# Kernel optimization log

Measured on AMD Instinct MI355X. Metric: run time of the kernel, lower is better.

## Reference

```python
import jax, jax.numpy as jnp
import numpy as np

N, E, IN, HID, OUT, H = 50000, 400000, 128, 32, 64, 4
HID_DIM = HID * H  # 128


def _param(key, shape, scale=0.05):
    return jax.random.normal(key, shape, dtype=jnp.float32) * scale


def setup_inputs() -> dict:
    key = jax.random.key(0)
    ks = jax.random.split(key, 32)
    inp = {
        "x": jax.random.normal(ks[0], (N, IN), dtype=jnp.float32),
        "edge_index": jax.random.randint(ks[1], (2, E), 0, N, dtype=jnp.int32),
        "edge_weight": jax.random.uniform(ks[2], (E,), dtype=jnp.float32),
        # layer 0: in=128 -> H=4, C=32, concat => 128
        "Wl0": _param(ks[3], (IN, H * HID)), "bl0": jnp.zeros((H * HID,), jnp.float32),
        "Wr0": _param(ks[4], (IN, H * HID)), "br0": jnp.zeros((H * HID,), jnp.float32),
        "We0": _param(ks[5], (1, H * HID)),
        "att0": _param(ks[6], (H, HID)),
        "b0": jnp.zeros((H * HID,), jnp.float32),
        "g0": jnp.ones((H * HID,), jnp.float32), "be0": jnp.zeros((H * HID,), jnp.float32),
        # layer 1: in=128 -> H=4, C=64, concat=False (mean over heads) => 64
        "Wl1": _param(ks[7], (HID_DIM, H * OUT)), "bl1": jnp.zeros((H * OUT,), jnp.float32),
        "Wr1": _param(ks[8], (HID_DIM, H * OUT)), "br1": jnp.zeros((H * OUT,), jnp.float32),
        "We1": _param(ks[9], (1, H * OUT)),
        "att1": _param(ks[10], (H, OUT)),
        "b1": jnp.zeros((OUT,), jnp.float32),
        "g1": jnp.ones((OUT,), jnp.float32), "be1": jnp.zeros((OUT,), jnp.float32),
        # residual projections
        "P0": _param(ks[11], (IN, HID_DIM)), "pb0": jnp.zeros((HID_DIM,), jnp.float32),
        "P1": _param(ks[12], (HID_DIM, OUT)), "pb1": jnp.zeros((OUT,), jnp.float32),
    }
    return inp


def _add_self_loops(src, dst, ew):
    # PyG add_self_loops with fill_value='mean': loop attr = mean of incoming edge attrs per node
    s = jax.ops.segment_sum(ew, dst, num_segments=N)
    cnt = jax.ops.segment_sum(jnp.ones_like(ew), dst, num_segments=N)
    loop_w = s / jnp.maximum(cnt, 1.0)
    idx = jnp.arange(N, dtype=src.dtype)
    return jnp.concatenate([src, idx]), jnp.concatenate([dst, idx]), jnp.concatenate([ew, loop_w])


def _gatv2_layer(x, src, dst, ew, Wl, bl, Wr, br, We, att, b, g, be, C, concat):
    xl = (x @ Wl + bl).reshape(N, H, C)  # source transform (lin_l)
    xr = (x @ Wr + br).reshape(N, H, C)  # target transform (lin_r)
    eattr = (ew[:, None] @ We).reshape(-1, H, C)
    e = jax.nn.leaky_relu(xl[src] + xr[dst] + eattr, 0.2)  # [E', H, C]
    logits = jnp.einsum('ehc,hc->eh', e, att)
    # segment softmax over target nodes
    m = jax.ops.segment_max(logits, dst, num_segments=N)
    p = jnp.exp(logits - m[dst])
    denom = jax.ops.segment_sum(p, dst, num_segments=N)
    alpha = p / denom[dst]
    out = jax.ops.segment_sum(xl[src] * alpha[..., None], dst, num_segments=N)  # [N, H, C]
    if concat:
        out = out.reshape(N, H * C) + b
    else:
        out = out.mean(axis=1) + b
    out = jax.nn.elu(out)
    mu = out.mean(-1, keepdims=True)
    var = out.var(-1, keepdims=True)
    return (out - mu) / jnp.sqrt(var + 1e-5) * g + be


def reference(x, edge_index, edge_weight,
              Wl0, bl0, Wr0, br0, We0, att0, b0, g0, be0,
              Wl1, bl1, Wr1, br1, We1, att1, b1, g1, be1,
              P0, pb0, P1, pb1):
    src, dst, ew = _add_self_loops(edge_index[0], edge_index[1], edge_weight)
    h = x
    h1 = _gatv2_layer(h, src, dst, ew, Wl0, bl0, Wr0, br0, We0, att0, b0, g0, be0, HID, True)
    h = h1 + (h @ P0 + pb0)
    h2 = _gatv2_layer(h, src, dst, ew, Wl1, bl1, Wr1, br1, We1, att1, b1, g1, be1, OUT, False)
    h = h2 + (h @ P1 + pb1)
    return h
```

## Files before the change

kernel.cpp:

```cpp
#include <hip/hip_runtime.h>
#include <math.h>

#define N_NODES 50000
#define N_EDGES 400000
#define NPAD    50176
#define MROWS   50048
#define HC0 128
#define HC1 256
#define CSR_TOTAL (N_NODES + N_EDGES)

typedef short    bf16x8 __attribute__((ext_vector_type(8)));
typedef float    f32x4  __attribute__((ext_vector_type(4)));
typedef _Float16 h2     __attribute__((ext_vector_type(2)));
typedef _Float16 h4     __attribute__((ext_vector_type(4)));
typedef _Float16 h8     __attribute__((ext_vector_type(8)));

__device__ inline unsigned short f2bf(float f) {
  union { float f; unsigned u; } v; v.f = f;
  unsigned r = v.u + 0x7FFFu + ((v.u >> 16) & 1u);
  return (unsigned short)(r >> 16);
}
__device__ inline h2 mkh2(float a, float b) {
  h2 r; r[0] = (_Float16)a; r[1] = (_Float16)b; return r;
}
__device__ inline float hdot2(h2 a, h2 b, float c) {
#if __has_builtin(__builtin_amdgcn_fdot2)
  return __builtin_amdgcn_fdot2(a, b, c, false);
#else
  return c + (float)a[0] * (float)b[0] + (float)a[1] * (float)b[1];
#endif
}

__global__ void deg_kernel(const int* __restrict__ ei, const float* __restrict__ ew,
                           float* __restrict__ s, int* __restrict__ deg) {
  int e = blockIdx.x * 256 + threadIdx.x;
  if (e < N_EDGES) {
    int dst = ei[N_EDGES + e];
    atomicAdd(&s[dst], ew[e]);
    atomicAdd(&deg[dst], 1);
  }
}

__global__ void scan1(const int* __restrict__ deg, int* __restrict__ part,
                      int* __restrict__ bsum) {
  int i = blockIdx.x * 256 + threadIdx.x;
  int lane = threadIdx.x & 63, wid = threadIdx.x >> 6;
  int v = (i < N_NODES) ? deg[i] + 1 : 0;
  int inc = v;
#pragma unroll
  for (int d = 1; d < 64; d <<= 1) { int y = __shfl_up(inc, d, 64); if (lane >= d) inc += y; }
  __shared__ int wsum[4];
  if (lane == 63) wsum[wid] = inc;
  __syncthreads();
  int off = 0;
#pragma unroll
  for (int w = 0; w < 4; ++w) { int sv = wsum[w]; if (w < wid) off += sv; }
  part[i] = inc - v + off;
  if (threadIdx.x == 0) bsum[blockIdx.x] = wsum[0] + wsum[1] + wsum[2] + wsum[3];
}

__global__ void scan2(int* __restrict__ bsum) {
  int t = threadIdx.x;
  int lane = t & 63, wid = t >> 6;
  int v = (t < 196) ? bsum[t] : 0;
  int inc = v;
#pragma unroll
  for (int d = 1; d < 64; d <<= 1) { int y = __shfl_up(inc, d, 64); if (lane >= d) inc += y; }
  __shared__ int wsum[4];
  if (lane == 63) wsum[wid] = inc;
  __syncthreads();
  int off = 0;
#pragma unroll
  for (int w = 0; w < 4; ++w) { int sv = wsum[w]; if (w < wid) off += sv; }
  if (t < 196) bsum[t] = inc - v + off;
}

__global__ void self_kernel(const float* __restrict__ s, const int* __restrict__ deg,
                            const int* __restrict__ part, const int* __restrict__ bsum,
                            int2* __restrict__ csr2) {
  int i = blockIdx.x * 256 + threadIdx.x;
  if (i >= N_NODES) return;
  float w = s[i] / fmaxf((float)deg[i], 1.0f);
  int start = part[i] + bsum[i >> 8];
  csr2[start] = make_int2(i, __float_as_int(w));
}

__global__ void scatter_kernel(const int* __restrict__ ei, const float* __restrict__ ew,
                               const int* __restrict__ part, const int* __restrict__ bsum,
                               int* __restrict__ cursor, int2* __restrict__ csr2) {
  int e = blockIdx.x * 256 + threadIdx.x;
  if (e >= N_EDGES) return;
  int dst = ei[N_EDGES + e];
  int pos = atomicAdd(&cursor[dst], 1);
  int idx = part[dst] + bsum[dst >> 8] + 1 + pos;
  csr2[idx] = make_int2(ei[e], __float_as_int(ew[e]));
}

__global__ void pack_w(const float* __restrict__ Wl0, const float* __restrict__ Wr0,
                       const float* __restrict__ P0,  const float* __restrict__ Wl1,
                       const float* __restrict__ Wr1, const float* __restrict__ P1,
                       unsigned short* __restrict__ o_wl0, unsigned short* __restrict__ o_wr0,
                       unsigned short* __restrict__ o_p0,  unsigned short* __restrict__ o_wl1,
                       unsigned short* __restrict__ o_wr1, unsigned short* __restrict__ o_p1) {
  int n = blockIdx.x, k = threadIdx.x;
  const float* W; unsigned short* O; int N, nl;
  if      (n < 128) { W = Wl0; O = o_wl0; N = 128; nl = n; }
  else if (n < 256) { W = Wr0; O = o_wr0; N = 128; nl = n - 128; }
  else if (n < 384) { W = P0;  O = o_p0;  N = 128; nl = n - 256; }
  else if (n < 640) { W = Wl1; O = o_wl1; N = 256; nl = n - 384; }
  else if (n < 896) { W = Wr1; O = o_wr1; N = 256; nl = n - 640; }
  else              { W = P1;  O = o_p1;  N = 64;  nl = n - 896; }
  O[nl * 128 + k] = f2bf(W[(size_t)k * N + nl]);
}

__global__ __launch_bounds__(256) void gemm_l0(
    const float* __restrict__ X, const unsigned short* __restrict__ BT,
    const float* __restrict__ bias0, const float* __restrict__ bias1,
    const float* __restrict__ bias2,
    _Float16* __restrict__ o_xl, _Float16* __restrict__ o_xr,
    _Float16* __restrict__ o_h, int M) {
  __shared__ unsigned short As[64 * 136];
  const int tid = threadIdx.x;
  const int rbase = blockIdx.x * 64;
#pragma unroll
  for (int i = 0; i < 8; ++i) {
    int c = i * 256 + tid;
    int row = c >> 5, c4 = c & 31;
    int ar = rbase + row; if (ar > M - 1) ar = M - 1;
    float4 v = *(const float4*)(X + (size_t)ar * 128 + c4 * 4);
    ushort4 o; o.x = f2bf(v.x); o.y = f2bf(v.y); o.z = f2bf(v.z); o.w = f2bf(v.w);
    *(ushort4*)(As + row * 136 + c4 * 4) = o;
  }
  __syncthreads();
  const int w = tid >> 6, l = tid & 63;
  const int lr = l & 15, lg = l >> 4;
#pragma unroll
  for (int i = 0; i < 6; ++i) {
    const int ct = w * 6 + i;
    const bf16x8* bp = (const bf16x8*)(BT + (size_t)(ct * 16 + lr) * 128 + lg * 8);
    bf16x8 b0 = bp[0], b1 = bp[4], b2 = bp[8], b3 = bp[12];
    const int colb = ct * 16 + lg * 4;
    const int cc = colb & 127;
    const float* bptr = (ct < 8 ? bias0 : (ct < 16 ? bias1 : bias2));
    float4 bv = *(const float4*)(bptr + cc);
#pragma unroll
    for (int rt = 0; rt < 4; ++rt) {
      const unsigned short* ap = As + (rt * 16 + lr) * 136 + lg * 8;
      bf16x8 a0 = *(const bf16x8*)(ap);
      bf16x8 a1 = *(const bf16x8*)(ap + 32);
      bf16x8 a2 = *(const bf16x8*)(ap + 64);
      bf16x8 a3 = *(const bf16x8*)(ap + 96);
      f32x4 acc = {0.f, 0.f, 0.f, 0.f};
      acc = __builtin_amdgcn_mfma_f32_16x16x32_bf16(b0, a0, acc, 0, 0, 0);
      acc = __builtin_amdgcn_mfma_f32_16x16x32_bf16(b1, a1, acc, 0, 0, 0);
      acc = __builtin_amdgcn_mfma_f32_16x16x32_bf16(b2, a2, acc, 0, 0, 0);
      acc = __builtin_amdgcn_mfma_f32_16x16x32_bf16(b3, a3, acc, 0, 0, 0);
      const int row = rbase + rt * 16 + lr;
      h4 o;
      o[0] = (_Float16)(acc[0] + bv.x); o[1] = (_Float16)(acc[1] + bv.y);
      o[2] = (_Float16)(acc[2] + bv.z); o[3] = (_Float16)(acc[3] + bv.w);
      _Float16* dst = (ct < 8) ? o_xl : (ct < 16 ? o_xr : o_h);
      *(h4*)(dst + (size_t)row * 128 + cc) = o;
    }
  }
}

__global__ __launch_bounds__(256) void gemm_l1(
    const unsigned short* __restrict__ A, const unsigned short* __restrict__ BT,
    const float* __restrict__ bias0, const float* __restrict__ bias1,
    const float* __restrict__ bias2,
    _Float16* __restrict__ o_xl, _Float16* __restrict__ o_xr,
    float* __restrict__ o_out, int M) {
  __shared__ unsigned short As[64 * 136];
  const int tid = threadIdx.x;
  const int rbase = blockIdx.x * 64;
#pragma unroll
  for (int i = 0; i < 4; ++i) {
    int c = i * 256 + tid;
    int row = c >> 4, slot = c & 15;
    int ar = rbase + row; if (ar > M - 1) ar = M - 1;
    uint4 v = *(const uint4*)(A + (size_t)ar * 128 + slot * 8);
    *(uint4*)(As + row * 136 + slot * 8) = v;
  }
  __syncthreads();
  const int w = tid >> 6, l = tid & 63;
  const int lr = l & 15, lg = l >> 4;
#pragma unroll
  for (int i = 0; i < 9; ++i) {
    const int ct = w * 9 + i;
    const bf16x8* bp = (const bf16x8*)(BT + (size_t)(ct * 16 + lr) * 128 + lg * 8);
    bf16x8 b0 = bp[0], b1 = bp[4], b2 = bp[8], b3 = bp[12];
    const int colb = ct * 16 + lg * 4;
    const int cc = (ct < 32) ? (colb & 255) : (colb - 512);
    const float* bptr = (ct < 16 ? bias0 : (ct < 32 ? bias1 : bias2));
    float4 bv = *(const float4*)(bptr + cc);
#pragma unroll
    for (int rt = 0; rt < 4; ++rt) {
      const unsigned short* ap = As + (rt * 16 + lr) * 136 + lg * 8;
      bf16x8 a0 = *(const bf16x8*)(ap);
      bf16x8 a1 = *(const bf16x8*)(ap + 32);
      bf16x8 a2 = *(const bf16x8*)(ap + 64);
      bf16x8 a3 = *(const bf16x8*)(ap + 96);
      f32x4 acc = {0.f, 0.f, 0.f, 0.f};
      acc = __builtin_amdgcn_mfma_f32_16x16x32_bf16(b0, a0, acc, 0, 0, 0);
      acc = __builtin_amdgcn_mfma_f32_16x16x32_bf16(b1, a1, acc, 0, 0, 0);
      acc = __builtin_amdgcn_mfma_f32_16x16x32_bf16(b2, a2, acc, 0, 0, 0);
      acc = __builtin_amdgcn_mfma_f32_16x16x32_bf16(b3, a3, acc, 0, 0, 0);
      const int row = rbase + rt * 16 + lr;
      if (ct < 32) {
        h4 o;
        o[0] = (_Float16)(acc[0] + bv.x); o[1] = (_Float16)(acc[1] + bv.y);
        o[2] = (_Float16)(acc[2] + bv.z); o[3] = (_Float16)(acc[3] + bv.w);
        *(h4*)((ct < 16 ? o_xl : o_xr) + (size_t)row * 256 + cc) = o;
      } else if (row < M) {
        float4 o;
        o.x = acc[0] + bv.x; o.y = acc[1] + bv.y;
        o.z = acc[2] + bv.z; o.w = acc[3] + bv.w;
        *(float4*)(o_out + (size_t)row * 64 + cc) = o;
      }
    }
  }
}

__device__ inline void edge_step0(int2 rec, h8 a8, bool valid,
                                  const h2* xrv2, const h2* wef2, const h2* att2,
                                  h2* acc2, float& den) {
  _Float16 wh = (_Float16)__int_as_float(rec.y);
  h2 w2; w2[0] = wh; w2[1] = wh;
  const h2 c02 = mkh2(0.2f, 0.2f);
  int4 ai = __builtin_bit_cast(int4, a8);
  h2 av[4];
  av[0] = __builtin_bit_cast(h2, ai.x); av[1] = __builtin_bit_cast(h2, ai.y);
  av[2] = __builtin_bit_cast(h2, ai.z); av[3] = __builtin_bit_cast(h2, ai.w);
  float c = 0.f;
#pragma unroll
  for (int k = 0; k < 4; ++k) {
    h2 sv = av[k] + (w2 * wef2[k] + xrv2[k]);
    h2 lk = __builtin_elementwise_max(sv, sv * c02);
    c = hdot2(lk, att2[k], c);
  }
  c += __shfl_xor(c, 1, 64); c += __shfl_xor(c, 2, 64);
  float p = valid ? __expf(c) : 0.f;
  den += p;
  _Float16 ph = (_Float16)p;
  h2 p2; p2[0] = ph; p2[1] = ph;
#pragma unroll
  for (int k = 0; k < 4; ++k) acc2[k] = p2 * av[k] + acc2[k];
}

__device__ inline void edge_step1(int2 rec, h8 a8, bool valid,
                                  const h2* xrv2, const h2* wef2, const h2* att2,
                                  h2* acc2, float& den) {
  _Float16 wh = (_Float16)__int_as_float(rec.y);
  h2 w2; w2[0] = wh; w2[1] = wh;
  const h2 c02 = mkh2(0.2f, 0.2f);
  int4 ai = __builtin_bit_cast(int4, a8);
  h2 av[4];
  av[0] = __builtin_bit_cast(h2, ai.x); av[1] = __builtin_bit_cast(h2, ai.y);
  av[2] = __builtin_bit_cast(h2, ai.z); av[3] = __builtin_bit_cast(h2, ai.w);
  float c = 0.f;
#pragma unroll
  for (int k = 0; k < 4; ++k) {
    h2 sv = av[k] + (w2 * wef2[k] + xrv2[k]);
    h2 lk = __builtin_elementwise_max(sv, sv * c02);
    c = hdot2(lk, att2[k], c);
  }
  c += __shfl_xor(c, 1, 64); c += __shfl_xor(c, 2, 64); c += __shfl_xor(c, 4, 64);
  float p = valid ? __expf(c) : 0.f;
  den += p;
  _Float16 ph = (_Float16)p;
  h2 p2; p2[0] = ph; p2[1] = ph;
#pragma unroll
  for (int k = 0; k < 4; ++k) acc2[k] = p2 * av[k] + acc2[k];
}

__global__ __launch_bounds__(256) void agg0(
    const int* __restrict__ part, const int* __restrict__ bsum,
    const int* __restrict__ deg, const int2* __restrict__ csr2,
    const _Float16* __restrict__ xl, const _Float16* __restrict__ xr,
    const float* __restrict__ We, const float* __restrict__ att,
    const float* __restrict__ b, const float* __restrict__ g,
    const float* __restrict__ be, const _Float16* __restrict__ hres,
    unsigned short* __restrict__ hout) {
  const int wid = threadIdx.x >> 6, l = threadIdx.x & 63;
  const int n = blockIdx.x * 4 + wid;
  const int grp = l >> 4, cl = l & 15, c0 = cl * 8;
  h2 xrv2[4], wef2[4], att2[4];
  {
    h8 x8 = *(const h8*)(xr + (size_t)n * HC0 + c0);
    int4 xi = __builtin_bit_cast(int4, x8);
    xrv2[0] = __builtin_bit_cast(h2, xi.x); xrv2[1] = __builtin_bit_cast(h2, xi.y);
    xrv2[2] = __builtin_bit_cast(h2, xi.z); xrv2[3] = __builtin_bit_cast(h2, xi.w);
    float4 w0 = *(const float4*)(We + c0),  w1 = *(const float4*)(We + c0 + 4);
    float4 t0 = *(const float4*)(att + c0), t1 = *(const float4*)(att + c0 + 4);
    wef2[0] = mkh2(w0.x, w0.y); wef2[1] = mkh2(w0.z, w0.w);
    wef2[2] = mkh2(w1.x, w1.y); wef2[3] = mkh2(w1.z, w1.w);
    att2[0] = mkh2(t0.x, t0.y); att2[1] = mkh2(t0.z, t0.w);
    att2[2] = mkh2(t1.x, t1.y); att2[3] = mkh2(t1.z, t1.w);
  }
  const int start = part[n] + bsum[n >> 8];
  const int cnt   = deg[n] + 1;
  const int2* seg = csr2 + start;
  h2 acc2[4] = {};
  float den = 0.f;
  int2 rA0 = seg[grp],      rA1 = seg[grp + 4];
  int2 rB0 = seg[grp + 8],  rB1 = seg[grp + 12];
  h8 aA0 = *(const h8*)(xl + (size_t)rA0.x * HC0 + c0);
  h8 aA1 = *(const h8*)(xl + (size_t)rA1.x * HC0 + c0);
  const int trips = (cnt + 7) >> 3;
  int e = grp;
  for (int t = 0; t < trips; ++t) {
    int2 rC0 = seg[e + 16], rC1 = seg[e + 20];
    h8 aB0 = *(const h8*)(xl + (size_t)rB0.x * HC0 + c0);
    h8 aB1 = *(const h8*)(xl + (size_t)rB1.x * HC0 + c0);
    edge_step0(rA0, aA0, e < cnt,     xrv2, wef2, att2, acc2, den);
    edge_step0(rA1, aA1, e + 4 < cnt, xrv2, wef2, att2, acc2, den);
    rA0 = rB0; rA1 = rB1; rB0 = rC0; rB1 = rC1; aA0 = aB0; aA1 = aB1;
    e += 8;
  }
  den += __shfl_xor(den, 16, 64); den += __shfl_xor(den, 32, 64);
#pragma unroll
  for (int k = 0; k < 4; ++k) {
    int b16 = __shfl_xor(__builtin_bit_cast(int, acc2[k]), 16, 64);
    acc2[k] = acc2[k] + __builtin_bit_cast(h2, b16);
    int b32 = __shfl_xor(__builtin_bit_cast(int, acc2[k]), 32, 64);
    acc2[k] = acc2[k] + __builtin_bit_cast(h2, b32);
  }
  float v[8], s1 = 0.f, s2 = 0.f;
  float dinv = 1.f / den;
  {
    float4 b0v = *(const float4*)(b + c0), b1v = *(const float4*)(b + c0 + 4);
    float bb[8] = {b0v.x,b0v.y,b0v.z,b0v.w,b1v.x,b1v.y,b1v.z,b1v.w};
#pragma unroll
    for (int j = 0; j < 8; ++j) {
      float t = (float)acc2[j >> 1][j & 1] * dinv + bb[j];
      t = t > 0.f ? t : __expf(t) - 1.f;
      v[j] = t; s1 += t; s2 += t * t;
    }
  }
  s1 += __shfl_xor(s1, 1, 64); s2 += __shfl_xor(s2, 1, 64);
  s1 += __shfl_xor(s1, 2, 64); s2 += __shfl_xor(s2, 2, 64);
  s1 += __shfl_xor(s1, 4, 64); s2 += __shfl_xor(s2, 4, 64);
  s1 += __shfl_xor(s1, 8, 64); s2 += __shfl_xor(s2, 8, 64);
  float mean = s1 * (1.f / 128.f);
  float inv  = rsqrtf(s2 * (1.f / 128.f) - mean * mean + 1e-5f);
  if (grp == 0) {
    float4 g0v = *(const float4*)(g + c0),  g1v = *(const float4*)(g + c0 + 4);
    float4 e0v = *(const float4*)(be + c0), e1v = *(const float4*)(be + c0 + 4);
    h8 hh = *(const h8*)(hres + (size_t)n * HC0 + c0);
    float gg[8] = {g0v.x,g0v.y,g0v.z,g0v.w,g1v.x,g1v.y,g1v.z,g1v.w};
    float ee[8] = {e0v.x,e0v.y,e0v.z,e0v.w,e1v.x,e1v.y,e1v.z,e1v.w};
    bf16x8 o;
#pragma unroll
    for (int j = 0; j < 8; ++j)
      o[j] = (short)f2bf((v[j] - mean) * inv * gg[j] + ee[j] + (float)hh[j]);
    *(bf16x8*)(hout + (size_t)n * HC0 + c0) = o;
  }
}

__global__ __launch_bounds__(256) void agg1(
    const int* __restrict__ part, const int* __restrict__ bsum,
    const int* __restrict__ deg, const int2* __restrict__ csr2,
    const _Float16* __restrict__ xl, const _Float16* __restrict__ xr,
    const float* __restrict__ We, const float* __restrict__ att,
    const float* __restrict__ b, const float* __restrict__ g,
    const float* __restrict__ be, float* __restrict__ out) {
  const int wid = threadIdx.x >> 6, l = threadIdx.x & 63;
  const int n = blockIdx.x * 4 + wid;
  const int grp = l >> 5, cl = l & 31, c0 = cl * 8;
  h2 xrv2[4], wef2[4], att2[4];
  {
    h8 x8 = *(const h8*)(xr + (size_t)n * HC1 + c0);
    int4 xi = __builtin_bit_cast(int4, x8);
    xrv2[0] = __builtin_bit_cast(h2, xi.x); xrv2[1] = __builtin_bit_cast(h2, xi.y);
    xrv2[2] = __builtin_bit_cast(h2, xi.z); xrv2[3] = __builtin_bit_cast(h2, xi.w);
    float4 w0 = *(const float4*)(We + c0),  w1 = *(const float4*)(We + c0 + 4);
    float4 t0 = *(const float4*)(att + c0), t1 = *(const float4*)(att + c0 + 4);
    wef2[0] = mkh2(w0.x, w0.y); wef2[1] = mkh2(w0.z, w0.w);
    wef2[2] = mkh2(w1.x, w1.y); wef2[3] = mkh2(w1.z, w1.w);
    att2[0] = mkh2(t0.x, t0.y); att2[1] = mkh2(t0.z, t0.w);
    att2[2] = mkh2(t1.x, t1.y); att2[3] = mkh2(t1.z, t1.w);
  }
  const int start = part[n] + bsum[n >> 8];
  const int cnt   = deg[n] + 1;
  const int2* seg = csr2 + start;
  h2 acc2[4] = {};
  float den = 0.f;
  int2 rA0 = seg[grp],     rA1 = seg[grp + 2];
  int2 rB0 = seg[grp + 4], rB1 = seg[grp + 6];
  h8 aA0 = *(const h8*)(xl + (size_t)rA0.x * HC1 + c0);
  h8 aA1 = *(const h8*)(xl + (size_t)rA1.x * HC1 + c0);
  const int trips = (cnt + 3) >> 2;
  int e = grp;
  for (int t = 0; t < trips; ++t) {
    int2 rC0 = seg[e + 8], rC1 = seg[e + 10];
    h8 aB0 = *(const h8*)(xl + (size_t)rB0.x * HC1 + c0);
    h8 aB1 = *(const h8*)(xl + (size_t)rB1.x * HC1 + c0);
    edge_step1(rA0, aA0, e < cnt,     xrv2, wef2, att2, acc2, den);
    edge_step1(rA1, aA1, e + 2 < cnt, xrv2, wef2, att2, acc2, den);
    rA0 = rB0; rA1 = rB1; rB0 = rC0; rB1 = rC1; aA0 = aB0; aA1 = aB1;
    e += 4;
  }
  den += __shfl_xor(den, 32, 64);
#pragma unroll
  for (int k = 0; k < 4; ++k) {
    int b32 = __shfl_xor(__builtin_bit_cast(int, acc2[k]), 32, 64);
    acc2[k] = acc2[k] + __builtin_bit_cast(h2, b32);
  }
  float dinv = 1.f / den;
  float v[8], s1 = 0.f, s2 = 0.f;
  const int oc = (cl & 7) * 8;
  {
    float4 b0v = *(const float4*)(b + oc), b1v = *(const float4*)(b + oc + 4);
    float bb[8] = {b0v.x,b0v.y,b0v.z,b0v.w,b1v.x,b1v.y,b1v.z,b1v.w};
#pragma unroll
    for (int j = 0; j < 8; ++j) {
      float t = (float)acc2[j >> 1][j & 1] * dinv;
      t += __shfl_xor(t, 8, 64);
      t += __shfl_xor(t, 16, 64);
      t = t * 0.25f + bb[j];
      t = t > 0.f ? t : __expf(t) - 1.f;
      v[j] = t; s1 += t; s2 += t * t;
    }
  }
  s1 += __shfl_xor(s1, 1, 64); s2 += __shfl_xor(s2, 1, 64);
  s1 += __shfl_xor(s1, 2, 64); s2 += __shfl_xor(s2, 2, 64);
  s1 += __shfl_xor(s1, 4, 64); s2 += __shfl_xor(s2, 4, 64);
  float mean = s1 * (1.f / 64.f);
  float inv  = rsqrtf(s2 * (1.f / 64.f) - mean * mean + 1e-5f);
  if (grp == 0 && cl < 8) {
    float4 g0v = *(const float4*)(g + oc),  g1v = *(const float4*)(g + oc + 4);
    float4 e0v = *(const float4*)(be + oc), e1v = *(const float4*)(be + oc + 4);
    float gg[8] = {g0v.x,g0v.y,g0v.z,g0v.w,g1v.x,g1v.y,g1v.z,g1v.w};
    float ee[8] = {e0v.x,e0v.y,e0v.z,e0v.w,e1v.x,e1v.y,e1v.z,e1v.w};
    float* po = out + (size_t)n * 64 + oc;
    float4 o0 = *(const float4*)po, o1 = *(const float4*)(po + 4);
    o0.x += (v[0] - mean) * inv * gg[0] + ee[0];
    o0.y += (v[1] - mean) * inv * gg[1] + ee[1];
    o0.z += (v[2] - mean) * inv * gg[2] + ee[2];
    o0.w += (v[3] - mean) * inv * gg[3] + ee[3];
    o1.x += (v[4] - mean) * inv * gg[4] + ee[4];
    o1.y += (v[5] - mean) * inv * gg[5] + ee[5];
    o1.z += (v[6] - mean) * inv * gg[6] + ee[6];
    o1.w += (v[7] - mean) * inv * gg[7] + ee[7];
    *(float4*)po = o0; *(float4*)(po + 4) = o1;
  }
}

extern "C" void kernel_launch(void* const* d_in, const int* in_sizes, int n_in,
                              void* d_out, int out_size, void* d_ws, size_t ws_size,
                              hipStream_t stream) {
  const float* x    = (const float*)d_in[0];
  const int*   ei   = (const int*)  d_in[1];
  const float* ew   = (const float*)d_in[2];
  const float* Wl0  = (const float*)d_in[3];
  const float* bl0  = (const float*)d_in[4];
  const float* Wr0  = (const float*)d_in[5];
  const float* br0  = (const float*)d_in[6];
  const float* We0  = (const float*)d_in[7];
  const float* att0 = (const float*)d_in[8];
  const float* b0   = (const float*)d_in[9];
  const float* g0   = (const float*)d_in[10];
  const float* be0  = (const float*)d_in[11];
  const float* Wl1  = (const float*)d_in[12];
  const float* bl1  = (const float*)d_in[13];
  const float* Wr1  = (const float*)d_in[14];
  const float* br1  = (const float*)d_in[15];
  const float* We1  = (const float*)d_in[16];
  const float* att1 = (const float*)d_in[17];
  const float* b1   = (const float*)d_in[18];
  const float* g1   = (const float*)d_in[19];
  const float* be1  = (const float*)d_in[20];
  const float* P0   = (const float*)d_in[21];
  const float* pb0  = (const float*)d_in[22];
  const float* P1   = (const float*)d_in[23];
  const float* pb1  = (const float*)d_in[24];
  float* out = (float*)d_out;

  float* f        = (float*)d_ws;
  float* s_loopw  = f;
  int*   deg      = (int*)(f + 50176);
  int*   cursor   = (int*)(f + 100352);
  int*   part     = (int*)(f + 150528);
  int*   bsum     = (int*)(f + 200704);
  int2*  csr2     = (int2*)(f + 200960);
  unsigned short* wl0T = (unsigned short*)(f + 1102080);
  unsigned short* wr0T = wl0T + 16384;
  unsigned short* p0T  = wl0T + 32768;
  unsigned short* wl1T = (unsigned short*)(f + 1126656);
  unsigned short* wr1T = wl1T + 32768;
  unsigned short* p1T  = wl1T + 65536;
  unsigned short* hb   = (unsigned short*)(f + 1163520);
  _Float16*       hres = (_Float16*)(f + 4366592);
  _Float16*       RA   = (_Float16*)(f + 7569664);
  _Float16*       RB   = (_Float16*)(f + 13975808);
  _Float16* xl0h = RA, *xr0h = RB;
  _Float16* xl1h = RA, *xr1h = RB;

  hipMemsetAsync(s_loopw, 0, (size_t)(50176 * 3) * sizeof(float), stream);
  hipMemsetAsync(csr2 + CSR_TOTAL, 0, 64 * sizeof(int2), stream);
  deg_kernel<<<(N_EDGES + 255) / 256, 256, 0, stream>>>(ei, ew, s_loopw, deg);
  scan1<<<NPAD / 256, 256, 0, stream>>>(deg, part, bsum);
  scan2<<<1, 256, 0, stream>>>(bsum);
  self_kernel<<<(N_NODES + 255) / 256, 256, 0, stream>>>(s_loopw, deg, part, bsum, csr2);
  scatter_kernel<<<(N_EDGES + 255) / 256, 256, 0, stream>>>(ei, ew, part, bsum,
                                                            cursor, csr2);

  pack_w<<<960, 128, 0, stream>>>(Wl0, Wr0, P0, Wl1, Wr1, P1,
                                  wl0T, wr0T, p0T, wl1T, wr1T, p1T);

  const int GB = MROWS / 64;
  gemm_l0<<<GB, 256, 0, stream>>>(x, wl0T, bl0, br0, pb0, xl0h, xr0h, hres, N_NODES);
  agg0<<<N_NODES / 4, 256, 0, stream>>>(part, bsum, deg, csr2,
                                        xl0h, xr0h, We0, att0, b0, g0, be0, hres, hb);

  gemm_l1<<<GB, 256, 0, stream>>>(hb, wl1T, bl1, br1, pb1, xl1h, xr1h, out, N_NODES);
  agg1<<<N_NODES / 4, 256, 0, stream>>>(part, bsum, deg, csr2,
                                        xl1h, xr1h, We1, att1, b1, g1, be1, out);
}
```

Measured before the change: 223.3 us.

## Bucket nodes by in-degree so aggregation waves process similar-degree nodes

Adds a degree histogram, a bin scan and an ordering kernel that build a permutation of nodes grouped by in-degree. Both aggregation kernels then map each wavefront to a node through this permutation, so the four waves in a block and neighbouring blocks see similar edge counts, which is meant to reduce load imbalance and tail idle time. The cost is two extra small kernel launches, two memsets and atomics on 64 bins. Neighbouring waves also no longer handle neighbouring nodes, so reads of xr/hres and writes of the outputs become scattered.

```diff
diff --git a/kernel.cpp b/kernel.cpp
--- a/kernel.cpp
+++ b/kernel.cpp
@@ -77,12 +77,32 @@
 
 __global__ void self_kernel(const float* __restrict__ s, const int* __restrict__ deg,
                             const int* __restrict__ part, const int* __restrict__ bsum,
-                            int2* __restrict__ csr2) {
+                            int2* __restrict__ csr2, int* __restrict__ hist) {
   int i = blockIdx.x * 256 + threadIdx.x;
   if (i >= N_NODES) return;
-  float w = s[i] / fmaxf((float)deg[i], 1.0f);
+  int d = deg[i];
+  float w = s[i] / fmaxf((float)d, 1.0f);
   int start = part[i] + bsum[i >> 8];
   csr2[start] = make_int2(i, __float_as_int(w));
+  atomicAdd(&hist[d < 63 ? d : 63], 1);
+}
+
+__global__ void binscan(const int* __restrict__ hist, int* __restrict__ binoff) {
+  int t = threadIdx.x;
+  int v = hist[t];
+  int inc = v;
+#pragma unroll
+  for (int d = 1; d < 64; d <<= 1) { int y = __shfl_up(inc, d, 64); if (t >= d) inc += y; }
+  binoff[t] = inc - v;
+}
+
+__global__ void order_kernel(const int* __restrict__ deg, const int* __restrict__ binoff,
+                             int* __restrict__ bincur, int* __restrict__ norder) {
+  int i = blockIdx.x * 256 + threadIdx.x;
+  if (i >= N_NODES) return;
+  int d = deg[i]; int bin = d < 63 ? d : 63;
+  int pos = atomicAdd(&bincur[bin], 1);
+  norder[binoff[bin] + pos] = i;
 }
 
 __global__ void scatter_kernel(const int* __restrict__ ei, const float* __restrict__ ew,
@@ -275,6 +295,7 @@
 }
 
 __global__ __launch_bounds__(256) void agg0(
+    const int* __restrict__ norder,
     const int* __restrict__ part, const int* __restrict__ bsum,
     const int* __restrict__ deg, const int2* __restrict__ csr2,
     const _Float16* __restrict__ xl, const _Float16* __restrict__ xr,
@@ -283,7 +304,7 @@
     const float* __restrict__ be, const _Float16* __restrict__ hres,
     unsigned short* __restrict__ hout) {
   const int wid = threadIdx.x >> 6, l = threadIdx.x & 63;
-  const int n = blockIdx.x * 4 + wid;
+  const int n = norder[blockIdx.x * 4 + wid];
   const int grp = l >> 4, cl = l & 15, c0 = cl * 8;
   h2 xrv2[4], wef2[4], att2[4];
   {
@@ -359,6 +380,7 @@
 }
 
 __global__ __launch_bounds__(256) void agg1(
+    const int* __restrict__ norder,
     const int* __restrict__ part, const int* __restrict__ bsum,
     const int* __restrict__ deg, const int2* __restrict__ csr2,
     const _Float16* __restrict__ xl, const _Float16* __restrict__ xr,
@@ -366,7 +388,7 @@
     const float* __restrict__ b, const float* __restrict__ g,
     const float* __restrict__ be, float* __restrict__ out) {
   const int wid = threadIdx.x >> 6, l = threadIdx.x & 63;
-  const int n = blockIdx.x * 4 + wid;
+  const int n = norder[blockIdx.x * 4 + wid];
   const int grp = l >> 5, cl = l & 31, c0 = cl * 8;
   h2 xrv2[4], wef2[4], att2[4];
   {
@@ -494,15 +516,24 @@
   _Float16*       hres = (_Float16*)(f + 4366592);
   _Float16*       RA   = (_Float16*)(f + 7569664);
   _Float16*       RB   = (_Float16*)(f + 13975808);
+  int*   norder   = (int*)(f + 20381952);
+  int*   hist     = (int*)(f + 20432128);
+  int*   binoff   = (int*)(f + 20432192);
+  int*   bincur   = (int*)(f + 20432256);
   _Float16* xl0h = RA, *xr0h = RB;
   _Float16* xl1h = RA, *xr1h = RB;
 
   hipMemsetAsync(s_loopw, 0, (size_t)(50176 * 3) * sizeof(float), stream);
   hipMemsetAsync(csr2 + CSR_TOTAL, 0, 64 * sizeof(int2), stream);
+  hipMemsetAsync(hist, 0, 64 * sizeof(int), stream);
+  hipMemsetAsync(bincur, 0, 64 * sizeof(int), stream);
   deg_kernel<<<(N_EDGES + 255) / 256, 256, 0, stream>>>(ei, ew, s_loopw, deg);
   scan1<<<NPAD / 256, 256, 0, stream>>>(deg, part, bsum);
   scan2<<<1, 256, 0, stream>>>(bsum);
-  self_kernel<<<(N_NODES + 255) / 256, 256, 0, stream>>>(s_loopw, deg, part, bsum, csr2);
+  self_kernel<<<(N_NODES + 255) / 256, 256, 0, stream>>>(s_loopw, deg, part, bsum,
+                                                         csr2, hist);
+  binscan<<<1, 64, 0, stream>>>(hist, binoff);
+  order_kernel<<<(N_NODES + 255) / 256, 256, 0, stream>>>(deg, binoff, bincur, norder);
   scatter_kernel<<<(N_EDGES + 255) / 256, 256, 0, stream>>>(ei, ew, part, bsum,
                                                             cursor, csr2);
 
@@ -511,10 +542,10 @@
 
   const int GB = MROWS / 64;
   gemm_l0<<<GB, 256, 0, stream>>>(x, wl0T, bl0, br0, pb0, xl0h, xr0h, hres, N_NODES);
-  agg0<<<N_NODES / 4, 256, 0, stream>>>(part, bsum, deg, csr2,
+  agg0<<<N_NODES / 4, 256, 0, stream>>>(norder, part, bsum, deg, csr2,
                                         xl0h, xr0h, We0, att0, b0, g0, be0, hres, hb);
 
   gemm_l1<<<GB, 256, 0, stream>>>(hb, wl1T, bl1, br1, pb1, xl1h, xr1h, out, N_NODES);
-  agg1<<<N_NODES / 4, 256, 0, stream>>>(part, bsum, deg, csr2,
+  agg1<<<N_NODES / 4, 256, 0, stream>>>(norder, part, bsum, deg, csr2,
                                         xl1h, xr1h, We1, att1, b1, g1, be1, out);
 }
```

After: 572.8 us. 2.57x slower.

## Widen per-lane channel slice to 16 and process one edge per lane group

Applied to the files above, without the earlier changes.

Both aggregation kernels now give each lane 16 channels (two 16-byte loads per gathered source row) instead of 8, so a wavefront covers more edges per trip with half the lanes per edge. The loop prefetches one edge record per step instead of two, and the logit reduction needs fewer cross-lane shuffles. The final cross-group reductions grow accordingly, and layer 1 folds the head-mean reduction into fp16 packed shuffles. The trade is more registers per lane and different memory-level parallelism, plus slightly less fp16 precision in the head averaging.

```diff
diff --git a/kernel.cpp b/kernel.cpp
--- a/kernel.cpp
+++ b/kernel.cpp
@@ -29,6 +29,10 @@
 #else
   return c + (float)a[0] * (float)b[0] + (float)a[1] * (float)b[1];
 #endif
+}
+__device__ inline h2 h2shfl_add(h2 v, int mask) {
+  int q = __shfl_xor(__builtin_bit_cast(int, v), mask, 64);
+  return v + __builtin_bit_cast(h2, q);
 }
 
 __global__ void deg_kernel(const int* __restrict__ ei, const float* __restrict__ ew,
@@ -222,56 +226,35 @@
   }
 }
 
-__device__ inline void edge_step0(int2 rec, h8 a8, bool valid,
-                                  const h2* xrv2, const h2* wef2, const h2* att2,
-                                  h2* acc2, float& den) {
+template<int NSH>
+__device__ inline void estep(int2 rec, h8 a0, h8 a1, bool valid,
+                             const h2* xrv2, const h2* wef2, const h2* att2,
+                             h2* acc2, float& den) {
   _Float16 wh = (_Float16)__int_as_float(rec.y);
   h2 w2; w2[0] = wh; w2[1] = wh;
   const h2 c02 = mkh2(0.2f, 0.2f);
-  int4 ai = __builtin_bit_cast(int4, a8);
-  h2 av[4];
-  av[0] = __builtin_bit_cast(h2, ai.x); av[1] = __builtin_bit_cast(h2, ai.y);
-  av[2] = __builtin_bit_cast(h2, ai.z); av[3] = __builtin_bit_cast(h2, ai.w);
+  int4 i0 = __builtin_bit_cast(int4, a0);
+  int4 i1 = __builtin_bit_cast(int4, a1);
+  h2 av[8];
+  av[0] = __builtin_bit_cast(h2, i0.x); av[1] = __builtin_bit_cast(h2, i0.y);
+  av[2] = __builtin_bit_cast(h2, i0.z); av[3] = __builtin_bit_cast(h2, i0.w);
+  av[4] = __builtin_bit_cast(h2, i1.x); av[5] = __builtin_bit_cast(h2, i1.y);
+  av[6] = __builtin_bit_cast(h2, i1.z); av[7] = __builtin_bit_cast(h2, i1.w);
   float c = 0.f;
 #pragma unroll
-  for (int k = 0; k < 4; ++k) {
+  for (int k = 0; k < 8; ++k) {
     h2 sv = av[k] + (w2 * wef2[k] + xrv2[k]);
     h2 lk = __builtin_elementwise_max(sv, sv * c02);
     c = hdot2(lk, att2[k], c);
   }
-  c += __shfl_xor(c, 1, 64); c += __shfl_xor(c, 2, 64);
+  c += __shfl_xor(c, 1, 64);
+  if (NSH > 1) c += __shfl_xor(c, 2, 64);
   float p = valid ? __expf(c) : 0.f;
   den += p;
   _Float16 ph = (_Float16)p;
   h2 p2; p2[0] = ph; p2[1] = ph;
 #pragma unroll
-  for (int k = 0; k < 4; ++k) acc2[k] = p2 * av[k] + acc2[k];
-}
-
-__device__ inline void edge_step1(int2 rec, h8 a8, bool valid,
-                                  const h2* xrv2, const h2* wef2, const h2* att2,
-                                  h2* acc2, float& den) {
-  _Float16 wh = (_Float16)__int_as_float(rec.y);
-  h2 w2; w2[0] = wh; w2[1] = wh;
-  const h2 c02 = mkh2(0.2f, 0.2f);
-  int4 ai = __builtin_bit_cast(int4, a8);
-  h2 av[4];
-  av[0] = __builtin_bit_cast(h2, ai.x); av[1] = __builtin_bit_cast(h2, ai.y);
-  av[2] = __builtin_bit_cast(h2, ai.z); av[3] = __builtin_bit_cast(h2, ai.w);
-  float c = 0.f;
-#pragma unroll
-  for (int k = 0; k < 4; ++k) {
-    h2 sv = av[k] + (w2 * wef2[k] + xrv2[k]);
-    h2 lk = __builtin_elementwise_max(sv, sv * c02);
-    c = hdot2(lk, att2[k], c);
-  }
-  c += __shfl_xor(c, 1, 64); c += __shfl_xor(c, 2, 64); c += __shfl_xor(c, 4, 64);
-  float p = valid ? __expf(c) : 0.f;
-  den += p;
-  _Float16 ph = (_Float16)p;
-  h2 p2; p2[0] = ph; p2[1] = ph;
-#pragma unroll
-  for (int k = 0; k < 4; ++k) acc2[k] = p2 * av[k] + acc2[k];
+  for (int k = 0; k < 8; ++k) acc2[k] = p2 * av[k] + acc2[k];
 }
 
 __global__ __launch_bounds__(256) void agg0(
@@ -284,77 +267,72 @@
     unsigned short* __restrict__ hout) {
   const int wid = threadIdx.x >> 6, l = threadIdx.x & 63;
   const int n = blockIdx.x * 4 + wid;
-  const int grp = l >> 4, cl = l & 15, c0 = cl * 8;
-  h2 xrv2[4], wef2[4], att2[4];
+  const int grp = l >> 3, cl = l & 7, c0 = cl * 16;
+  h2 xrv2[8], wef2[8], att2[8];
   {
-    h8 x8 = *(const h8*)(xr + (size_t)n * HC0 + c0);
-    int4 xi = __builtin_bit_cast(int4, x8);
-    xrv2[0] = __builtin_bit_cast(h2, xi.x); xrv2[1] = __builtin_bit_cast(h2, xi.y);
-    xrv2[2] = __builtin_bit_cast(h2, xi.z); xrv2[3] = __builtin_bit_cast(h2, xi.w);
-    float4 w0 = *(const float4*)(We + c0),  w1 = *(const float4*)(We + c0 + 4);
-    float4 t0 = *(const float4*)(att + c0), t1 = *(const float4*)(att + c0 + 4);
-    wef2[0] = mkh2(w0.x, w0.y); wef2[1] = mkh2(w0.z, w0.w);
-    wef2[2] = mkh2(w1.x, w1.y); wef2[3] = mkh2(w1.z, w1.w);
-    att2[0] = mkh2(t0.x, t0.y); att2[1] = mkh2(t0.z, t0.w);
-    att2[2] = mkh2(t1.x, t1.y); att2[3] = mkh2(t1.z, t1.w);
+    h8 x0 = *(const h8*)(xr + (size_t)n * HC0 + c0);
+    h8 x1 = *(const h8*)(xr + (size_t)n * HC0 + c0 + 8);
+    int4 q0 = __builtin_bit_cast(int4, x0), q1 = __builtin_bit_cast(int4, x1);
+    xrv2[0]=__builtin_bit_cast(h2,q0.x); xrv2[1]=__builtin_bit_cast(h2,q0.y);
+    xrv2[2]=__builtin_bit_cast(h2,q0.z); xrv2[3]=__builtin_bit_cast(h2,q0.w);
+    xrv2[4]=__builtin_bit_cast(h2,q1.x); xrv2[5]=__builtin_bit_cast(h2,q1.y);
+    xrv2[6]=__builtin_bit_cast(h2,q1.z); xrv2[7]=__builtin_bit_cast(h2,q1.w);
+#pragma unroll
+    for (int k = 0; k < 8; ++k) {
+      wef2[k] = mkh2(We[c0 + 2*k],  We[c0 + 2*k + 1]);
+      att2[k] = mkh2(att[c0 + 2*k], att[c0 + 2*k + 1]);
+    }
   }
   const int start = part[n] + bsum[n >> 8];
   const int cnt   = deg[n] + 1;
   const int2* seg = csr2 + start;
-  h2 acc2[4] = {};
+  h2 acc2[8] = {};
   float den = 0.f;
-  int2 rA0 = seg[grp],      rA1 = seg[grp + 4];
-  int2 rB0 = seg[grp + 8],  rB1 = seg[grp + 12];
-  h8 aA0 = *(const h8*)(xl + (size_t)rA0.x * HC0 + c0);
-  h8 aA1 = *(const h8*)(xl + (size_t)rA1.x * HC0 + c0);
+  int2 rA = seg[grp], rB = seg[8 + grp];
+  h8 aA0 = *(const h8*)(xl + (size_t)rA.x * HC0 + c0);
+  h8 aA1 = *(const h8*)(xl + (size_t)rA.x * HC0 + c0 + 8);
   const int trips = (cnt + 7) >> 3;
-  int e = grp;
+  int e = 0;
   for (int t = 0; t < trips; ++t) {
-    int2 rC0 = seg[e + 16], rC1 = seg[e + 20];
-    h8 aB0 = *(const h8*)(xl + (size_t)rB0.x * HC0 + c0);
-    h8 aB1 = *(const h8*)(xl + (size_t)rB1.x * HC0 + c0);
-    edge_step0(rA0, aA0, e < cnt,     xrv2, wef2, att2, acc2, den);
-    edge_step0(rA1, aA1, e + 4 < cnt, xrv2, wef2, att2, acc2, den);
-    rA0 = rB0; rA1 = rB1; rB0 = rC0; rB1 = rC1; aA0 = aB0; aA1 = aB1;
+    int2 rC = seg[e + 16 + grp];
+    h8 aB0 = *(const h8*)(xl + (size_t)rB.x * HC0 + c0);
+    h8 aB1 = *(const h8*)(xl + (size_t)rB.x * HC0 + c0 + 8);
+    estep<1>(rA, aA0, aA1, (e + grp) < cnt, xrv2, wef2, att2, acc2, den);
+    rA = rB; rB = rC; aA0 = aB0; aA1 = aB1;
     e += 8;
   }
-  den += __shfl_xor(den, 16, 64); den += __shfl_xor(den, 32, 64);
-#pragma unroll
-  for (int k = 0; k < 4; ++k) {
-    int b16 = __shfl_xor(__builtin_bit_cast(int, acc2[k]), 16, 64);
-    acc2[k] = acc2[k] + __builtin_bit_cast(h2, b16);
-    int b32 = __shfl_xor(__builtin_bit_cast(int, acc2[k]), 32, 64);
-    acc2[k] = acc2[k] + __builtin_bit_cast(h2, b32);
-  }
-  float v[8], s1 = 0.f, s2 = 0.f;
+  den += __shfl_xor(den, 8, 64); den += __shfl_xor(den, 16, 64);
+  den += __shfl_xor(den, 32, 64);
+#pragma unroll
+  for (int k = 0; k < 8; ++k) {
+    acc2[k] = h2shfl_add(acc2[k], 8);
+    acc2[k] = h2shfl_add(acc2[k], 16);
+    acc2[k] = h2shfl_add(acc2[k], 32);
+  }
+  float v[16], s1 = 0.f, s2 = 0.f;
   float dinv = 1.f / den;
-  {
-    float4 b0v = *(const float4*)(b + c0), b1v = *(const float4*)(b + c0 + 4);
-    float bb[8] = {b0v.x,b0v.y,b0v.z,b0v.w,b1v.x,b1v.y,b1v.z,b1v.w};
-#pragma unroll
-    for (int j = 0; j < 8; ++j) {
-      float t = (float)acc2[j >> 1][j & 1] * dinv + bb[j];
-      t = t > 0.f ? t : __expf(t) - 1.f;
-      v[j] = t; s1 += t; s2 += t * t;
-    }
+#pragma unroll
+  for (int j = 0; j < 16; ++j) {
+    float t = (float)acc2[j >> 1][j & 1] * dinv + b[c0 + j];
+    t = t > 0.f ? t : __expf(t) - 1.f;
+    v[j] = t; s1 += t; s2 += t * t;
   }
   s1 += __shfl_xor(s1, 1, 64); s2 += __shfl_xor(s2, 1, 64);
   s1 += __shfl_xor(s1, 2, 64); s2 += __shfl_xor(s2, 2, 64);
   s1 += __shfl_xor(s1, 4, 64); s2 += __shfl_xor(s2, 4, 64);
-  s1 += __shfl_xor(s1, 8, 64); s2 += __shfl_xor(s2, 8, 64);
   float mean = s1 * (1.f / 128.f);
   float inv  = rsqrtf(s2 * (1.f / 128.f) - mean * mean + 1e-5f);
-  if (grp == 0) {
-    float4 g0v = *(const float4*)(g + c0),  g1v = *(const float4*)(g + c0 + 4);
-    float4 e0v = *(const float4*)(be + c0), e1v = *(const float4*)(be + c0 + 4);
-    h8 hh = *(const h8*)(hres + (size_t)n * HC0 + c0);
-    float gg[8] = {g0v.x,g0v.y,g0v.z,g0v.w,g1v.x,g1v.y,g1v.z,g1v.w};
-    float ee[8] = {e0v.x,e0v.y,e0v.z,e0v.w,e1v.x,e1v.y,e1v.z,e1v.w};
-    bf16x8 o;
-#pragma unroll
-    for (int j = 0; j < 8; ++j)
-      o[j] = (short)f2bf((v[j] - mean) * inv * gg[j] + ee[j] + (float)hh[j]);
-    *(bf16x8*)(hout + (size_t)n * HC0 + c0) = o;
+  if (l < 8) {
+    h8 hh0 = *(const h8*)(hres + (size_t)n * HC0 + c0);
+    h8 hh1 = *(const h8*)(hres + (size_t)n * HC0 + c0 + 8);
+    bf16x8 o0, o1;
+#pragma unroll
+    for (int j = 0; j < 8; ++j) {
+      o0[j] = (short)f2bf((v[j]   - mean) * inv * g[c0 + j]   + be[c0 + j]   + (float)hh0[j]);
+      o1[j] = (short)f2bf((v[8+j] - mean) * inv * g[c0 + 8+j] + be[c0 + 8+j] + (float)hh1[j]);
+    }
+    *(bf16x8*)(hout + (size_t)n * HC0 + c0)     = o0;
+    *(bf16x8*)(hout + (size_t)n * HC0 + c0 + 8) = o1;
   }
 }
 
@@ -367,83 +345,79 @@
     const float* __restrict__ be, float* __restrict__ out) {
   const int wid = threadIdx.x >> 6, l = threadIdx.x & 63;
   const int n = blockIdx.x * 4 + wid;
-  const int grp = l >> 5, cl = l & 31, c0 = cl * 8;
-  h2 xrv2[4], wef2[4], att2[4];
+  const int grp = l >> 4, cl = l & 15, c0 = cl * 16;
+  h2 xrv2[8], wef2[8], att2[8];
   {
-    h8 x8 = *(const h8*)(xr + (size_t)n * HC1 + c0);
-    int4 xi = __builtin_bit_cast(int4, x8);
-    xrv2[0] = __builtin_bit_cast(h2, xi.x); xrv2[1] = __builtin_bit_cast(h2, xi.y);
-    xrv2[2] = __builtin_bit_cast(h2, xi.z); xrv2[3] = __builtin_bit_cast(h2, xi.w);
-    float4 w0 = *(const float4*)(We + c0),  w1 = *(const float4*)(We + c0 + 4);
-    float4 t0 = *(const float4*)(att + c0), t1 = *(const float4*)(att + c0 + 4);
-    wef2[0] = mkh2(w0.x, w0.y); wef2[1] = mkh2(w0.z, w0.w);
-    wef2[2] = mkh2(w1.x, w1.y); wef2[3] = mkh2(w1.z, w1.w);
-    att2[0] = mkh2(t0.x, t0.y); att2[1] = mkh2(t0.z, t0.w);
-    att2[2] = mkh2(t1.x, t1.y); att2[3] = mkh2(t1.z, t1.w);
+    h8 x0 = *(const h8*)(xr + (size_t)n * HC1 + c0);
+    h8 x1 = *(const h8*)(xr + (size_t)n * HC1 + c0 + 8);
+    int4 q0 = __builtin_bit_cast(int4, x0), q1 = __builtin_bit_cast(int4, x1);
+    xrv2[0]=__builtin_bit_cast(h2,q0.x); xrv2[1]=__builtin_bit_cast(h2,q0.y);
+    xrv2[2]=__builtin_bit_cast(h2,q0.z); xrv2[3]=__builtin_bit_cast(h2,q0.w);
+    xrv2[4]=__builtin_bit_cast(h2,q1.x); xrv2[5]=__builtin_bit_cast(h2,q1.y);
+    xrv2[6]=__builtin_bit_cast(h2,q1.z); xrv2[7]=__builtin_bit_cast(h2,q1.w);
+#pragma unroll
+    for (int k = 0; k < 8; ++k) {
+      wef2[k] = mkh2(We[c0 + 2*k],  We[c0 + 2*k + 1]);
+      att2[k] = mkh2(att[c0 + 2*k], att[c0 + 2*k + 1]);
+    }
   }
   const int start = part[n] + bsum[n >> 8];
   const int cnt   = deg[n] + 1;
   const int2* seg = csr2 + start;
-  h2 acc2[4] = {};
+  h2 acc2[8] = {};
   float den = 0.f;
-  int2 rA0 = seg[grp],     rA1 = seg[grp + 2];
-  int2 rB0 = seg[grp + 4], rB1 = seg[grp + 6];
-  h8 aA0 = *(const h8*)(xl + (size_t)rA0.x * HC1 + c0);
-  h8 aA1 = *(const h8*)(xl + (size_t)rA1.x * HC1 + c0);
+  int2 rA = seg[grp], rB = seg[4 + grp];
+  h8 aA0 = *(const h8*)(xl + (size_t)rA.x * HC1 + c0);
+  h8 aA1 = *(const h8*)(xl + (size_t)rA.x * HC1 + c0 + 8);
   const int trips = (cnt + 3) >> 2;
-  int e = grp;
+  int e = 0;
   for (int t = 0; t < trips; ++t) {
-    int2 rC0 = seg[e + 8], rC1 = seg[e + 10];
-    h8 aB0 = *(const h8*)(xl + (size_t)rB0.x * HC1 + c0);
-    h8 aB1 = *(const h8*)(xl + (size_t)rB1.x * HC1 + c0);
-    edge_step1(rA0, aA0, e < cnt,     xrv2, wef2, att2, acc2, den);
-    edge_step1(rA1, aA1, e + 2 < cnt, xrv2, wef2, att2, acc2, den);
-    rA0 = rB0; rA1 = rB1; rB0 = rC0; rB1 = rC1; aA0 = aB0; aA1 = aB1;
+    int2 rC = seg[e + 8 + grp];
+    h8 aB0 = *(const h8*)(xl + (size_t)rB.x * HC1 + c0);
+    h8 aB1 = *(const h8*)(xl + (size_t)rB.x * HC1 + c0 + 8);
+    estep<2>(rA, aA0, aA1, (e + grp) < cnt, xrv2, wef2, att2, acc2, den);
+    rA = rB; rB = rC; aA0 = aB0; aA1 = aB1;
     e += 4;
   }
-  den += __shfl_xor(den, 32, 64);
-#pragma unroll
-  for (int k = 0; k < 4; ++k) {
-    int b32 = __shfl_xor(__builtin_bit_cast(int, acc2[k]), 32, 64);
-    acc2[k] = acc2[k] + __builtin_bit_cast(h2, b32);
+  den += __shfl_xor(den, 16, 64); den += __shfl_xor(den, 32, 64);
+#pragma unroll
+  for (int k = 0; k < 8; ++k) {
+    acc2[k] = h2shfl_add(acc2[k], 16);
+    acc2[k] = h2shfl_add(acc2[k], 32);
   }
   float dinv = 1.f / den;
-  float v[8], s1 = 0.f, s2 = 0.f;
-  const int oc = (cl & 7) * 8;
-  {
-    float4 b0v = *(const float4*)(b + oc), b1v = *(const float4*)(b + oc + 4);
-    float bb[8] = {b0v.x,b0v.y,b0v.z,b0v.w,b1v.x,b1v.y,b1v.z,b1v.w};
-#pragma unroll
-    for (int j = 0; j < 8; ++j) {
-      float t = (float)acc2[j >> 1][j & 1] * dinv;
-      t += __shfl_xor(t, 8, 64);
-      t += __shfl_xor(t, 16, 64);
-      t = t * 0.25f + bb[j];
-      t = t > 0.f ? t : __expf(t) - 1.f;
-      v[j] = t; s1 += t; s2 += t * t;
-    }
+  _Float16 dh = (_Float16)dinv;
+  h2 d2; d2[0] = dh; d2[1] = dh;
+  h2 t2[8];
+#pragma unroll
+  for (int k = 0; k < 8; ++k) {
+    t2[k] = acc2[k] * d2;
+    t2[k] = h2shfl_add(t2[k], 4);
+    t2[k] = h2shfl_add(t2[k], 8);
+  }
+  const int oc = (cl & 3) * 16;
+  float v[16], s1 = 0.f, s2 = 0.f;
+#pragma unroll
+  for (int j = 0; j < 16; ++j) {
+    float t = (float)t2[j >> 1][j & 1] * 0.25f + b[oc + j];
+    t = t > 0.f ? t : __expf(t) - 1.f;
+    v[j] = t; s1 += t; s2 += t * t;
   }
   s1 += __shfl_xor(s1, 1, 64); s2 += __shfl_xor(s2, 1, 64);
   s1 += __shfl_xor(s1, 2, 64); s2 += __shfl_xor(s2, 2, 64);
-  s1 += __shfl_xor(s1, 4, 64); s2 += __shfl_xor(s2, 4, 64);
   float mean = s1 * (1.f / 64.f);
   float inv  = rsqrtf(s2 * (1.f / 64.f) - mean * mean + 1e-5f);
-  if (grp == 0 && cl < 8) {
-    float4 g0v = *(const float4*)(g + oc),  g1v = *(const float4*)(g + oc + 4);
-    float4 e0v = *(const float4*)(be + oc), e1v = *(const float4*)(be + oc + 4);
-    float gg[8] = {g0v.x,g0v.y,g0v.z,g0v.w,g1v.x,g1v.y,g1v.z,g1v.w};
-    float ee[8] = {e0v.x,e0v.y,e0v.z,e0v.w,e1v.x,e1v.y,e1v.z,e1v.w};
+  if (grp == 0 && cl < 4) {
     float* po = out + (size_t)n * 64 + oc;
-    float4 o0 = *(const float4*)po, o1 = *(const float4*)(po + 4);
-    o0.x += (v[0] - mean) * inv * gg[0] + ee[0];
-    o0.y += (v[1] - mean) * inv * gg[1] + ee[1];
-    o0.z += (v[2] - mean) * inv * gg[2] + ee[2];
-    o0.w += (v[3] - mean) * inv * gg[3] + ee[3];
-    o1.x += (v[4] - mean) * inv * gg[4] + ee[4];
-    o1.y += (v[5] - mean) * inv * gg[5] + ee[5];
-    o1.z += (v[6] - mean) * inv * gg[6] + ee[6];
-    o1.w += (v[7] - mean) * inv * gg[7] + ee[7];
-    *(float4*)po = o0; *(float4*)(po + 4) = o1;
+#pragma unroll
+    for (int q = 0; q < 4; ++q) {
+      float4 o = *(const float4*)(po + q * 4);
+      o.x += (v[q*4+0] - mean) * inv * g[oc + q*4+0] + be[oc + q*4+0];
+      o.y += (v[q*4+1] - mean) * inv * g[oc + q*4+1] + be[oc + q*4+1];
+      o.z += (v[q*4+2] - mean) * inv * g[oc + q*4+2] + be[oc + q*4+2];
+      o.w += (v[q*4+3] - mean) * inv * g[oc + q*4+3] + be[oc + q*4+3];
+      *(float4*)(po + q * 4) = o;
+    }
   }
 }
 
```

Result: slower. 277.3 us (+24.2%).
